# Kernel tuning notes

Measured on AMD Instinct MI355X. Metric: run time of the kernel, lower is better.

## Reference

```python
import jax, jax.numpy as jnp
import numpy as np

EPS = 1e-5  # torch LayerNorm default
NUM_HEADS = 12


def layer_norm(x, g, b):
    m = jnp.mean(x, axis=-1, keepdims=True)
    v = jnp.var(x, axis=-1, keepdims=True)
    return (x - m) * jax.lax.rsqrt(v + EPS) * g + b


def split_heads(x):
    B, N, C = x.shape
    return x.reshape(B, N, NUM_HEADS, C // NUM_HEADS).transpose(0, 2, 1, 3)  # [B,H,N,D]


def merge_heads(x):
    B, H, N, D = x.shape
    return x.transpose(0, 2, 1, 3).reshape(B, N, H * D)


def attn_core(q, k, v, mask):
    # q:[B,H,Nq,D], k/v:[B,H,Nk,D], mask:[B,Nk] float (1=keep)
    d = q.shape[-1]
    scores = jnp.einsum('bhqd,bhkd->bhqk', q, k) * (d ** -0.5)
    scores = scores + (1.0 - mask)[:, None, None, :] * -5.0
    a = jax.nn.softmax(scores, axis=-1)
    return jnp.einsum('bhqk,bhkd->bhqd', a, v)


def setup_inputs() -> dict:
    key = jax.random.key(0)
    B, N, C = 4, 1024, 768
    Hd = C * 4  # mlp hidden = 3072
    ks = jax.random.split(key, 12)
    s = 0.02
    inp = {
        'x': jax.random.normal(ks[0], (B, N, C), jnp.float32),
        'encoder_out': jax.random.normal(ks[1], (B, N, C), jnp.float32),
        'mask': jnp.ones((B, N), jnp.float32),
        'encoder_mask': jnp.ones((B, N), jnp.float32),
        'ln1_g': jnp.ones((C,), jnp.float32), 'ln1_b': jnp.zeros((C,), jnp.float32),
        'qkv_w': jax.random.normal(ks[2], (C, 3 * C), jnp.float32) * s,
        'sa_proj_w': jax.random.normal(ks[3], (C, C), jnp.float32) * s,
        'sa_proj_b': jnp.zeros((C,), jnp.float32),
        'ln2_g': jnp.ones((C,), jnp.float32), 'ln2_b': jnp.zeros((C,), jnp.float32),
        'q_w': jax.random.normal(ks[4], (C, C), jnp.float32) * s,
        'kv_w': jax.random.normal(ks[5], (C, 2 * C), jnp.float32) * s,
        'ca_proj_w': jax.random.normal(ks[6], (C, C), jnp.float32) * s,
        'ca_proj_b': jnp.zeros((C,), jnp.float32),
        'ln3_g': jnp.ones((C,), jnp.float32), 'ln3_b': jnp.zeros((C,), jnp.float32),
        'fc1_w': jax.random.normal(ks[7], (C, Hd), jnp.float32) * s,
        'fc1_b': jnp.zeros((Hd,), jnp.float32),
        'fc2_w': jax.random.normal(ks[8], (Hd, C), jnp.float32) * s,
        'fc2_b': jnp.zeros((C,), jnp.float32),
    }
    return inp


def reference(x, encoder_out, mask, encoder_mask,
              ln1_g, ln1_b, qkv_w, sa_proj_w, sa_proj_b,
              ln2_g, ln2_b, q_w, kv_w, ca_proj_w, ca_proj_b,
              ln3_g, ln3_b, fc1_w, fc1_b, fc2_w, fc2_b):
    B, N, C = x.shape
    D = C // NUM_HEADS
    # --- self attention ---
    h = layer_norm(x, ln1_g, ln1_b)
    qkv = (h @ qkv_w).reshape(B, N, 3, NUM_HEADS, D)
    q = qkv[:, :, 0].transpose(0, 2, 1, 3)
    k = qkv[:, :, 1].transpose(0, 2, 1, 3)
    v = qkv[:, :, 2].transpose(0, 2, 1, 3)
    o = merge_heads(attn_core(q, k, v, mask)) @ sa_proj_w + sa_proj_b
    x = x + o
    # --- cross attention ---
    h = layer_norm(x, ln2_g, ln2_b)
    q = split_heads(h @ q_w)
    Be, Ne, Ce = encoder_out.shape
    kv = (encoder_out @ kv_w).reshape(Be, Ne, 2, NUM_HEADS, D)
    k = kv[:, :, 0].transpose(0, 2, 1, 3)
    v = kv[:, :, 1].transpose(0, 2, 1, 3)
    o = merge_heads(attn_core(q, k, v, encoder_mask)) @ ca_proj_w + ca_proj_b
    x = x + o
    # --- MLP (exact GELU, like torch nn.GELU default) ---
    h = layer_norm(x, ln3_g, ln3_b)
    h = jax.nn.gelu(h @ fc1_w + fc1_b, approximate=False) @ fc2_w + fc2_b
    return x + h
```

## Files before the change

kernel.cpp:

```cpp
#include <hip/hip_runtime.h>

typedef __attribute__((ext_vector_type(8))) __bf16 bf16x8;
typedef __attribute__((ext_vector_type(4))) float f32x4;

__device__ __forceinline__ void gload_lds16(const __bf16* g, __bf16* l) {
    __builtin_amdgcn_global_load_lds(
        (const __attribute__((address_space(1))) void*)g,
        (__attribute__((address_space(3))) void*)l,
        16, 0, 0);
}

__global__ void transpose_f2b(const float* __restrict__ in, __bf16* __restrict__ outp,
                              int R, int Ccols) {
    __shared__ __bf16 tile[32][33];
    int bx = blockIdx.x * 32, by = blockIdx.y * 32;
    int tx = threadIdx.x & 31, ty = threadIdx.x >> 5;
#pragma unroll
    for (int i = ty; i < 32; i += 8)
        tile[i][tx] = (__bf16)in[(size_t)(by + i) * Ccols + bx + tx];
    __syncthreads();
#pragma unroll
    for (int i = ty; i < 32; i += 8)
        outp[(size_t)(bx + i) * R + by + tx] = tile[tx][i];
}

__global__ void cvt_f2b(const float* __restrict__ in, __bf16* __restrict__ outp) {
    int i = blockIdx.x * blockDim.x + threadIdx.x;
    float4 v = ((const float4*)in)[i];
    __bf16 o4[4] = {(__bf16)v.x, (__bf16)v.y, (__bf16)v.z, (__bf16)v.w};
    *(uint2*)(outp + (size_t)i * 4) = *(const uint2*)o4;
}

__global__ __launch_bounds__(256) void ln_kernel(const float* __restrict__ x,
                                                 const float* __restrict__ g,
                                                 const float* __restrict__ b,
                                                 __bf16* __restrict__ o) {
    int row = blockIdx.x, tid = threadIdx.x;
    const float* xr = x + (size_t)row * 768;
    float v0 = xr[tid], v1 = xr[tid + 256], v2 = xr[tid + 512];
    float s = v0 + v1 + v2, s2 = v0 * v0 + v1 * v1 + v2 * v2;
#pragma unroll
    for (int d = 32; d >= 1; d >>= 1) {
        s += __shfl_xor(s, d);
        s2 += __shfl_xor(s2, d);
    }
    __shared__ float red[8];
    int wave = tid >> 6, lane = tid & 63;
    if (!lane) { red[wave] = s; red[4 + wave] = s2; }
    __syncthreads();
    s = red[0] + red[1] + red[2] + red[3];
    s2 = red[4] + red[5] + red[6] + red[7];
    float mean = s * (1.0f / 768.0f);
    float var = s2 * (1.0f / 768.0f) - mean * mean;
    float inv = rsqrtf(var + 1e-5f);
    o[(size_t)row * 768 + tid]       = (__bf16)((v0 - mean) * inv * g[tid]       + b[tid]);
    o[(size_t)row * 768 + tid + 256] = (__bf16)((v1 - mean) * inv * g[tid + 256] + b[tid + 256]);
    o[(size_t)row * 768 + tid + 512] = (__bf16)((v2 - mean) * inv * g[tid + 512] + b[tid + 512]);
}

template <int BM, int BIAS, int RESID, int GELU, typename TO>
__global__ __launch_bounds__(256, 2) void gemm_nt(
    const __bf16* __restrict__ A, int lda,
    const __bf16* __restrict__ Bt, int ldb,
    TO* __restrict__ C, int ldc,
    const float* __restrict__ bias,
    const float* __restrict__ resid,
    int K) {
    __shared__ __bf16 lA[2][BM * 32];
    __shared__ __bf16 lB[2][128 * 32];
    constexpr int WCOLS = 256 / BM;
    constexpr int NF = (BM == 128) ? 4 : 2;
    constexpr int WNSP = (BM == 128) ? 64 : 32;
    const int tid = threadIdx.x;
    const int wave = tid >> 6, lane = tid & 63;
    const int wm = wave / WCOLS, wn = wave % WCOLS;
    const int bn = blockIdx.x * 128, bm = blockIdx.y * BM;
    const int ln15 = lane & 15, hi = lane >> 4;

    f32x4 acc[4][NF] = {};

    const int srow = tid >> 2;
    const int scol = (((tid & 3) ^ (srow & 3)) * 8);
    const __bf16* gA0 = A + (size_t)(bm + srow) * lda + scol;
    const __bf16* gA1 = A + (size_t)(bm + 64 + srow) * lda + scol;
    const __bf16* gB0 = Bt + (size_t)(bn + srow) * ldb + scol;
    const __bf16* gB1 = Bt + (size_t)(bn + 64 + srow) * ldb + scol;

    const int rswz = (hi * 8) ^ ((lane & 3) * 8);
    const int rAoff = (wm * 64 + ln15) * 32 + rswz;
    const int rBoff = (wn * WNSP + ln15) * 32 + rswz;

    auto STAGE = [&](int buf, int k0) {
        gload_lds16(gA0 + k0, lA[buf] + wave * 512);
        if constexpr (BM == 128) gload_lds16(gA1 + k0, lA[buf] + 2048 + wave * 512);
        gload_lds16(gB0 + k0, lB[buf] + wave * 512);
        gload_lds16(gB1 + k0, lB[buf] + 2048 + wave * 512);
    };
    auto COMPUTE = [&](int buf) {
        const __bf16* rA = lA[buf] + rAoff;
        const __bf16* rB = lB[buf] + rBoff;
        bf16x8 af[4], bfr[NF];
#pragma unroll
        for (int m = 0; m < 4; ++m) af[m] = *(const bf16x8*)(rA + m * 512);
#pragma unroll
        for (int n = 0; n < NF; ++n) bfr[n] = *(const bf16x8*)(rB + n * 512);
#pragma unroll
        for (int m = 0; m < 4; ++m)
#pragma unroll
            for (int n = 0; n < NF; ++n)
                acc[m][n] = __builtin_amdgcn_mfma_f32_16x16x32_bf16(af[m], bfr[n], acc[m][n], 0, 0, 0);
    };

    const int nt = K >> 5;
    STAGE(0, 0);
    for (int t = 0; t < nt - 1; ++t) {
        const int cur = t & 1;
        STAGE(cur ^ 1, (t + 1) << 5);
        if constexpr (BM == 128) asm volatile("s_waitcnt vmcnt(4)" ::: "memory");
        else                     asm volatile("s_waitcnt vmcnt(3)" ::: "memory");
        __builtin_amdgcn_s_barrier();
        __builtin_amdgcn_sched_barrier(0);
        COMPUTE(cur);
        __builtin_amdgcn_sched_barrier(0);
        __builtin_amdgcn_s_barrier();
    }
    asm volatile("s_waitcnt vmcnt(0)" ::: "memory");
    __builtin_amdgcn_s_barrier();
    __builtin_amdgcn_sched_barrier(0);
    COMPUTE((nt - 1) & 1);

#pragma unroll
    for (int m = 0; m < 4; ++m)
#pragma unroll
        for (int n = 0; n < NF; ++n)
#pragma unroll
            for (int r = 0; r < 4; ++r) {
                int row = bm + wm * 64 + m * 16 + hi * 4 + r;
                int col = bn + wn * WNSP + n * 16 + ln15;
                float v = acc[m][n][r];
                if (BIAS) v += bias[col];
                if (GELU) v = 0.5f * v * (1.0f + erff(v * 0.70710678118f));
                if (RESID) v += resid[(size_t)row * ldc + col];
                C[(size_t)row * ldc + col] = (TO)v;
            }
}

__global__ __launch_bounds__(256, 2) void attn_kernel(
    const __bf16* __restrict__ Qp, int ldq, int qcol,
    const __bf16* __restrict__ Kp, int ldk, int kcol,
    const __bf16* __restrict__ Vp, int ldv, int vcol,
    const float* __restrict__ mask,
    __bf16* __restrict__ Out) {
    __shared__ __bf16 lK[64 * 64];
    __shared__ __bf16 lV[64 * 64];
    __shared__ __bf16 lP[4][16 * 64];
    const int tid = threadIdx.x, wave = tid >> 6, lane = tid & 63;
    const int bh = blockIdx.y, b = bh / 12, h = bh % 12;
    const int qt = blockIdx.x;
    const int ln15 = lane & 15, hi = lane >> 4;

    const __bf16* qrow = Qp + (size_t)(b * 1024 + qt * 64 + wave * 16 + ln15) * ldq + qcol + h * 64;
    bf16x8 qf0 = *(const bf16x8*)(qrow + hi * 8);
    bf16x8 qf1 = *(const bf16x8*)(qrow + 32 + hi * 8);

    float l_part[4] = {0.f, 0.f, 0.f, 0.f};
    f32x4 oacc[4] = {};

    const int skey = tid >> 3;
    const int ssrc = (((tid & 7) ^ (skey & 7)) * 8);
    const __bf16* gK = Kp + (size_t)(b * 1024 + skey) * ldk + kcol + h * 64 + ssrc;
    __bf16* lK0 = lK + wave * 512;
    __bf16* lK1 = lK + 2048 + wave * 512;

    const int vkey = tid & 63;
    const int vdb = wave * 16;
    const __bf16* gV = Vp + (size_t)(b * 1024 + vkey) * ldv + vcol + h * 64 + vdb;

    const int kswz = (lane & 7) * 8;
    const __bf16* rK = lK + ln15 * 64;
    const __bf16* rV = lV + ln15 * 64;
    __bf16* wP = lP[wave];
    const __bf16* rP = lP[wave] + ln15 * 64;

    const float C1 = 0.18033688f;
    for (int kt = 0; kt < 16; ++kt) {
        const size_t tb = (size_t)kt * 64;
        gload_lds16(gK + tb * ldk, lK0);
        gload_lds16(gK + (tb + 32) * ldk, lK1);
        bf16x8 v0 = *(const bf16x8*)(gV + tb * ldv);
        bf16x8 v1 = *(const bf16x8*)(gV + tb * ldv + 8);
#pragma unroll
        for (int j = 0; j < 8; ++j) {
            lV[(vdb + j) * 64 + (vkey ^ (j * 8))] = v0[j];
            lV[(vdb + 8 + j) * 64 + (vkey ^ (j * 8))] = v1[j];
        }
        __syncthreads();

        f32x4 s[4];
#pragma unroll
        for (int n = 0; n < 4; ++n) {
            bf16x8 kf0 = *(const bf16x8*)(rK + n * 1024 + ((hi * 8) ^ kswz));
            bf16x8 kf1 = *(const bf16x8*)(rK + n * 1024 + ((hi * 8 + 32) ^ kswz));
            f32x4 z = {};
            z = __builtin_amdgcn_mfma_f32_16x16x32_bf16(qf0, kf0, z, 0, 0, 0);
            s[n] = __builtin_amdgcn_mfma_f32_16x16x32_bf16(qf1, kf1, z, 0, 0, 0);
        }
        float mb2[4];
#pragma unroll
        for (int n = 0; n < 4; ++n)
            mb2[n] = (1.0f - mask[b * 1024 + kt * 64 + n * 16 + ln15]) * -7.2134752f;

#pragma unroll
        for (int n = 0; n < 4; ++n)
#pragma unroll
            for (int r = 0; r < 4; ++r) {
                s[n][r] = exp2f(s[n][r] * C1 + mb2[n]);
                l_part[r] += s[n][r];
            }

#pragma unroll
        for (int n = 0; n < 4; ++n)
#pragma unroll
            for (int r = 0; r < 4; ++r) {
                int prow = hi * 4 + r;
                wP[prow * 64 + ((n * 16 + ln15) ^ ((prow & 7) * 8))] = (__bf16)s[n][r];
            }
        bf16x8 pf0 = *(const bf16x8*)(rP + ((hi * 8) ^ kswz));
        bf16x8 pf1 = *(const bf16x8*)(rP + ((hi * 8 + 32) ^ kswz));
#pragma unroll
        for (int n = 0; n < 4; ++n) {
            bf16x8 vf0 = *(const bf16x8*)(rV + n * 1024 + ((hi * 8) ^ kswz));
            bf16x8 vf1 = *(const bf16x8*)(rV + n * 1024 + ((hi * 8 + 32) ^ kswz));
            oacc[n] = __builtin_amdgcn_mfma_f32_16x16x32_bf16(pf0, vf0, oacc[n], 0, 0, 0);
            oacc[n] = __builtin_amdgcn_mfma_f32_16x16x32_bf16(pf1, vf1, oacc[n], 0, 0, 0);
        }
        __syncthreads();
    }

#pragma unroll
    for (int r = 0; r < 4; ++r) {
#pragma unroll
        for (int d = 1; d < 16; d <<= 1) l_part[r] += __shfl_xor(l_part[r], d);
        l_part[r] = 1.0f / l_part[r];
    }

#pragma unroll
    for (int n = 0; n < 4; ++n)
#pragma unroll
        for (int r = 0; r < 4; ++r) {
            int row = b * 1024 + qt * 64 + wave * 16 + hi * 4 + r;
            int col = h * 64 + n * 16 + ln15;
            Out[(size_t)row * 768 + col] = (__bf16)(oacc[n][r] * l_part[r]);
        }
}

extern "C" void kernel_launch(void* const* d_in, const int* in_sizes, int n_in,
                              void* d_out, int out_size, void* d_ws, size_t ws_size,
                              hipStream_t stream) {
    const float* x     = (const float*)d_in[0];
    const float* enc   = (const float*)d_in[1];
    const float* mask  = (const float*)d_in[2];
    const float* emask = (const float*)d_in[3];
    const float* ln1_g = (const float*)d_in[4];
    const float* ln1_b = (const float*)d_in[5];
    const float* qkv_w = (const float*)d_in[6];
    const float* sa_w  = (const float*)d_in[7];
    const float* sa_b  = (const float*)d_in[8];
    const float* ln2_g = (const float*)d_in[9];
    const float* ln2_b = (const float*)d_in[10];
    const float* q_w   = (const float*)d_in[11];
    const float* kv_w  = (const float*)d_in[12];
    const float* ca_w  = (const float*)d_in[13];
    const float* ca_b  = (const float*)d_in[14];
    const float* ln3_g = (const float*)d_in[15];
    const float* ln3_b = (const float*)d_in[16];
    const float* fc1_w = (const float*)d_in[17];
    const float* fc1_b = (const float*)d_in[18];
    const float* fc2_w = (const float*)d_in[19];
    const float* fc2_b = (const float*)d_in[20];
    float* out = (float*)d_out;

    char* w = (char*)d_ws;
    size_t off = 0;
    auto alloc = [&](size_t bytes) { void* p = w + off; off += bytes; return p; };
    __bf16* qkv_t = (__bf16*)alloc((size_t)2304 * 768 * 2);
    __bf16* sa_t  = (__bf16*)alloc((size_t)768 * 768 * 2);
    __bf16* q_t   = (__bf16*)alloc((size_t)768 * 768 * 2);
    __bf16* kv_t  = (__bf16*)alloc((size_t)1536 * 768 * 2);
    __bf16* ca_t  = (__bf16*)alloc((size_t)768 * 768 * 2);
    __bf16* fc1_t = (__bf16*)alloc((size_t)3072 * 768 * 2);
    __bf16* fc2_t = (__bf16*)alloc((size_t)768 * 3072 * 2);
    __bf16* H     = (__bf16*)alloc((size_t)4096 * 768 * 2);
    __bf16* QKV   = (__bf16*)alloc((size_t)4096 * 2304 * 2);
    __bf16* ATT   = (__bf16*)alloc((size_t)4096 * 768 * 2);
    float*  X1    = (float*)alloc((size_t)4096 * 768 * 4);
    float*  X2    = (float*)alloc((size_t)4096 * 768 * 4);
    __bf16* encb  = (__bf16*)alloc((size_t)4096 * 768 * 2);
    __bf16* HID   = QKV;
    __bf16* Qb    = QKV;
    __bf16* KVb   = QKV + (size_t)4096 * 768;

    dim3 blk(256);
    transpose_f2b<<<dim3(72, 24), blk, 0, stream>>>(qkv_w, qkv_t, 768, 2304);
    transpose_f2b<<<dim3(24, 24), blk, 0, stream>>>(sa_w, sa_t, 768, 768);
    transpose_f2b<<<dim3(24, 24), blk, 0, stream>>>(q_w, q_t, 768, 768);
    transpose_f2b<<<dim3(48, 24), blk, 0, stream>>>(kv_w, kv_t, 768, 1536);
    transpose_f2b<<<dim3(24, 24), blk, 0, stream>>>(ca_w, ca_t, 768, 768);
    transpose_f2b<<<dim3(96, 24), blk, 0, stream>>>(fc1_w, fc1_t, 768, 3072);
    transpose_f2b<<<dim3(24, 96), blk, 0, stream>>>(fc2_w, fc2_t, 3072, 768);
    cvt_f2b<<<dim3(3072), blk, 0, stream>>>(enc, encb);

    ln_kernel<<<4096, blk, 0, stream>>>(x, ln1_g, ln1_b, H);
    gemm_nt<128, 0, 0, 0, __bf16><<<dim3(18, 32), blk, 0, stream>>>(H, 768, qkv_t, 768, QKV, 2304, nullptr, nullptr, 768);
    attn_kernel<<<dim3(16, 48), blk, 0, stream>>>(QKV, 2304, 0, QKV, 2304, 768, QKV, 2304, 1536, mask, ATT);
    gemm_nt<64, 1, 1, 0, float><<<dim3(6, 64), blk, 0, stream>>>(ATT, 768, sa_t, 768, X1, 768, sa_b, x, 768);
    ln_kernel<<<4096, blk, 0, stream>>>(X1, ln2_g, ln2_b, H);
    gemm_nt<64, 0, 0, 0, __bf16><<<dim3(6, 64), blk, 0, stream>>>(H, 768, q_t, 768, Qb, 768, nullptr, nullptr, 768);
    gemm_nt<128, 0, 0, 0, __bf16><<<dim3(12, 32), blk, 0, stream>>>(encb, 768, kv_t, 768, KVb, 1536, nullptr, nullptr, 768);
    attn_kernel<<<dim3(16, 48), blk, 0, stream>>>(Qb, 768, 0, KVb, 1536, 0, KVb, 1536, 768, emask, ATT);
    gemm_nt<64, 1, 1, 0, float><<<dim3(6, 64), blk, 0, stream>>>(ATT, 768, ca_t, 768, X2, 768, ca_b, X1, 768);
    ln_kernel<<<4096, blk, 0, stream>>>(X2, ln3_g, ln3_b, H);
    gemm_nt<128, 1, 0, 1, __bf16><<<dim3(24, 32), blk, 0, stream>>>(H, 768, fc1_t, 768, HID, 3072, fc1_b, nullptr, 768);
    gemm_nt<64, 1, 1, 0, float><<<dim3(6, 64), blk, 0, stream>>>(HID, 3072, fc2_t, 3072, out, 768, fc2_b, X2, 3072);
}
```

Measured before the change: 438.3 us.

## Deepen GEMM LDS pipeline to four stages and change LDS swizzle

The bf16 GEMM's double-buffered LDS staging becomes a four-buffer ring that keeps three k-tiles of global-to-LDS loads in flight, with vmcnt waits sized per tile variant and an explicit three-step drain. This is meant to hide more global memory latency behind MFMA work. The LDS XOR swizzle now keys on (row>>1)&3 instead of row&3, presumably to cut bank conflicts on the fragment reads. LDS use doubles, which may lower occupancy below the two blocks per CU set in the launch bounds.

```diff
diff --git a/kernel.cpp b/kernel.cpp
--- a/kernel.cpp
+++ b/kernel.cpp
@@ -9,6 +9,12 @@
         (__attribute__((address_space(3))) void*)l,
         16, 0, 0);
 }
+
+template <int N> struct WaitVm;
+#define WV(n) template <> struct WaitVm<n> { static __device__ __forceinline__ void run() { \
+    asm volatile("s_waitcnt vmcnt(" #n ")" ::: "memory"); } };
+WV(0) WV(3) WV(4) WV(6) WV(8) WV(9) WV(12)
+#undef WV
 
 __global__ void transpose_f2b(const float* __restrict__ in, __bf16* __restrict__ outp,
                               int R, int Ccols) {
@@ -66,8 +72,9 @@
     const float* __restrict__ bias,
     const float* __restrict__ resid,
     int K) {
-    __shared__ __bf16 lA[2][BM * 32];
-    __shared__ __bf16 lB[2][128 * 32];
+    __shared__ __bf16 lA[4][BM * 32];
+    __shared__ __bf16 lB[4][128 * 32];
+    constexpr int L = (BM == 128) ? 4 : 3;
     constexpr int WCOLS = 256 / BM;
     constexpr int NF = (BM == 128) ? 4 : 2;
     constexpr int WNSP = (BM == 128) ? 64 : 32;
@@ -80,13 +87,13 @@
     f32x4 acc[4][NF] = {};
 
     const int srow = tid >> 2;
-    const int scol = (((tid & 3) ^ (srow & 3)) * 8);
+    const int scol = (((tid & 3) ^ ((srow >> 1) & 3)) * 8);
     const __bf16* gA0 = A + (size_t)(bm + srow) * lda + scol;
     const __bf16* gA1 = A + (size_t)(bm + 64 + srow) * lda + scol;
     const __bf16* gB0 = Bt + (size_t)(bn + srow) * ldb + scol;
     const __bf16* gB1 = Bt + (size_t)(bn + 64 + srow) * ldb + scol;
 
-    const int rswz = (hi * 8) ^ ((lane & 3) * 8);
+    const int rswz = (hi * 8) ^ (((ln15 >> 1) & 3) * 8);
     const int rAoff = (wm * 64 + ln15) * 32 + rswz;
     const int rBoff = (wn * WNSP + ln15) * 32 + rswz;
 
@@ -113,21 +120,33 @@
 
     const int nt = K >> 5;
     STAGE(0, 0);
-    for (int t = 0; t < nt - 1; ++t) {
-        const int cur = t & 1;
-        STAGE(cur ^ 1, (t + 1) << 5);
-        if constexpr (BM == 128) asm volatile("s_waitcnt vmcnt(4)" ::: "memory");
-        else                     asm volatile("s_waitcnt vmcnt(3)" ::: "memory");
+    STAGE(1, 32);
+    STAGE(2, 64);
+    for (int t = 0; t < nt - 3; ++t) {
+        STAGE((t + 3) & 3, (t + 3) << 5);
+        WaitVm<3 * L>::run();
         __builtin_amdgcn_s_barrier();
         __builtin_amdgcn_sched_barrier(0);
-        COMPUTE(cur);
+        COMPUTE(t & 3);
         __builtin_amdgcn_sched_barrier(0);
         __builtin_amdgcn_s_barrier();
     }
-    asm volatile("s_waitcnt vmcnt(0)" ::: "memory");
-    __builtin_amdgcn_s_barrier();
-    __builtin_amdgcn_sched_barrier(0);
-    COMPUTE((nt - 1) & 1);
+    WaitVm<2 * L>::run();
+    __builtin_amdgcn_s_barrier();
+    __builtin_amdgcn_sched_barrier(0);
+    COMPUTE((nt - 3) & 3);
+    __builtin_amdgcn_sched_barrier(0);
+    __builtin_amdgcn_s_barrier();
+    WaitVm<L>::run();
+    __builtin_amdgcn_s_barrier();
+    __builtin_amdgcn_sched_barrier(0);
+    COMPUTE((nt - 2) & 3);
+    __builtin_amdgcn_sched_barrier(0);
+    __builtin_amdgcn_s_barrier();
+    WaitVm<0>::run();
+    __builtin_amdgcn_s_barrier();
+    __builtin_amdgcn_sched_barrier(0);
+    COMPUTE((nt - 1) & 3);
 
 #pragma unroll
     for (int m = 0; m < 4; ++m)
```

Result: slower. 457.5 us (+4.4%).
